# Kernel optimization log

Measured on AMD Instinct MI355X. Metric: run time of the kernel, lower is better.

Reference implementation:

```python
import jax, jax.numpy as jnp
import numpy as np

EPS = 1e-5
NEG_SLOPE = 0.01  # torch F.leaky_relu default


def _batchnorm(h, gamma, beta):
    # BatchNorm1d in training mode: batch stats over node dim, biased variance
    mu = jnp.mean(h, axis=0)
    var = jnp.mean((h - mu) ** 2, axis=0)
    return gamma * (h - mu) * jax.lax.rsqrt(var + EPS) + beta


def setup_inputs() -> dict:
    N, E, H, ED = 16384, 524288, 128, 16
    key = jax.random.key(0)
    ks = jax.random.split(key, 12)
    s = 1.0 / np.sqrt(H)
    return {
        "x": jax.random.normal(ks[0], (N, H), jnp.float32),
        "edge_index": jax.random.randint(ks[1], (2, E), 0, N, jnp.int64),
        "edge_attr": jax.random.normal(ks[2], (E, ED), jnp.float32),
        "Wq": jax.random.normal(ks[3], (H, H), jnp.float32) * s,
        "bq": jnp.zeros((H,), jnp.float32),
        "Wk": jax.random.normal(ks[4], (H, H), jnp.float32) * s,
        "bk": jnp.zeros((H,), jnp.float32),
        "Wv": jax.random.normal(ks[5], (H, H), jnp.float32) * s,
        "bv": jnp.zeros((H,), jnp.float32),
        "We": jax.random.normal(ks[6], (ED, 1), jnp.float32) * (1.0 / np.sqrt(ED)),
        "be": jnp.zeros((1,), jnp.float32),
        "bn1_g": jnp.ones((H,), jnp.float32),
        "bn1_b": jnp.zeros((H,), jnp.float32),
        "W1": jax.random.normal(ks[7], (H, 2 * H), jnp.float32) * s,
        "b1": jnp.zeros((2 * H,), jnp.float32),
        "W2": jax.random.normal(ks[8], (2 * H, H), jnp.float32) * (1.0 / np.sqrt(2 * H)),
        "b2": jnp.zeros((H,), jnp.float32),
        "bn2_g": jnp.ones((H,), jnp.float32),
        "bn2_b": jnp.zeros((H,), jnp.float32),
    }


def reference(x, edge_index, edge_attr, Wq, bq, Wk, bk, Wv, bv, We, be,
              bn1_g, bn1_b, W1, b1, W2, b2, bn2_g, bn2_b):
    N = x.shape[0]
    Q = x @ Wq + bq  # [N, H]
    K = x @ Wk + bk
    V = x @ Wv + bv
    Ebias = (edge_attr @ We + be)[:, 0]  # [E], num_heads == 1
    src, dst = edge_index[0], edge_index[1]
    # per-edge dot product over the FULL hidden dim (as in the source)
    scores = jnp.sum(Q[src] * K[dst], axis=1) + Ebias  # [E]
    scores = jnp.where(scores >= 0, scores, NEG_SLOPE * scores)
    # to_dense_adj scatter-adds edge_attr into a dense [N, N] adjacency
    adj = jnp.zeros((N, N), x.dtype).at[src, dst].add(scores)
    attn = jax.nn.softmax(adj, axis=1)  # dense softmax incl. zero non-edges
    x_new = attn @ V  # [N, H]
    h = _batchnorm(x + x_new, bn1_g, bn1_b)
    ffn = jax.nn.relu(h @ W1 + b1) @ W2 + b2
    return _batchnorm(h + ffn, bn2_g, bn2_b)
```

## Files before the change

kernel.cpp:

```cpp
#include <hip/hip_runtime.h>
#include <hip/hip_bf16.h>
#include <math.h>

#define H 128
#define H2 256
#define SLAB 96
#define LDA 136
#define LDA2 264
#define EPS 1e-5f

typedef __attribute__((ext_vector_type(8))) short s16x8;
typedef __attribute__((ext_vector_type(4))) float f32x4;

__device__ __forceinline__ unsigned short f2bf(float f) {
  unsigned u = __float_as_uint(f);
  unsigned r = (u + 0x7FFFu + ((u >> 16) & 1u)) >> 16;
  return (unsigned short)r;
}
__device__ __forceinline__ float bf2f(unsigned short s) {
  return __uint_as_float(((unsigned)s) << 16);
}
__device__ __forceinline__ unsigned short f2h(float f) {
  union { unsigned short s; _Float16 h; } c; c.h = (_Float16)f; return c.s;
}
__device__ __forceinline__ float h2f(unsigned short u) {
  union { unsigned short s; _Float16 h; } c; c.s = u; return (float)c.h;
}

__global__ void wprep(const float* __restrict__ Wq, const float* __restrict__ Wk,
                      const float* __restrict__ Wv, const float* __restrict__ W1,
                      const float* __restrict__ W2,
                      short* qh, short* kh, short* vh, short* w1h, short* w2h,
                      int* __restrict__ cnt, float* __restrict__ stats, int N)
{
  int job = blockIdx.z;
  if (job == 5) {
    int t = blockIdx.x * 256 + threadIdx.x;
    if (t < N) cnt[t] = 0;
    if (t < 72 * H) stats[t] = 0.f;
    return;
  }
  const float* src; short* dh; int Kd, Nn; bool ashalf;
  if (job == 0)      { src = Wq; dh = qh;  Kd = 128; Nn = 128; ashalf = true; }
  else if (job == 1) { src = Wk; dh = kh;  Kd = 128; Nn = 128; ashalf = true; }
  else if (job == 2) { src = Wv; dh = vh;  Kd = 128; Nn = 128; ashalf = true; }
  else if (job == 3) { src = W1; dh = w1h; Kd = 128; Nn = 256; ashalf = false; }
  else               { src = W2; dh = w2h; Kd = 256; Nn = 128; ashalf = false; }
  int t = blockIdx.x * 256 + threadIdx.x;
  if (t >= Kd * Nn) return;
  int n = t / Kd, k = t - n * Kd;
  float v = src[(size_t)k * Nn + n];
  dh[t] = ashalf ? (short)f2h(v) : (short)f2bf(v);
}

__global__ __launch_bounds__(256) void qkv_mfma(
    const float* __restrict__ x,
    const short* __restrict__ Wqh, const short* __restrict__ Wkh,
    const short* __restrict__ Wvh,
    const float* __restrict__ bq, const float* __restrict__ bk,
    const float* __restrict__ bv,
    unsigned short* __restrict__ Qh, unsigned short* __restrict__ Kh,
    unsigned short* __restrict__ Vh, float* __restrict__ SVp,
    const float* __restrict__ ea, const float* __restrict__ We,
    const float* __restrict__ be, float* __restrict__ Eb,
    int E, int nqkv)
{
  __shared__ __align__(16) short A[64 * LDA];
  int tid = threadIdx.x;

  if (blockIdx.x >= nqkv) {
    int e = (blockIdx.x - nqkv) * 256 + tid;
    if (e < E) {
      float4 w0 = *(const float4*)&We[0], w1 = *(const float4*)&We[4];
      float4 w2 = *(const float4*)&We[8], w3 = *(const float4*)&We[12];
      const float4* p = (const float4*)&ea[(size_t)e * 16];
      float4 a0 = p[0], a1 = p[1], a2 = p[2], a3 = p[3];
      float s = a0.x * w0.x + a0.y * w0.y + a0.z * w0.z + a0.w * w0.w
              + a1.x * w1.x + a1.y * w1.y + a1.z * w1.z + a1.w * w1.w
              + a2.x * w2.x + a2.y * w2.y + a2.z * w2.z + a2.w * w2.w
              + a3.x * w3.x + a3.y * w3.y + a3.z * w3.z + a3.w * w3.w;
      Eb[e] = s + be[0];
    }
    return;
  }

  int bm = blockIdx.x * 64;
  int wave = tid >> 6, lane = tid & 63;
  int quad = lane >> 4, l16 = lane & 15;
  int wn = wave * 32;

#pragma unroll
  for (int i = 0; i < 4; ++i) {
    int g = i * 256 + tid;
    int row = g >> 4, f = g & 15;
    const float4* xp = (const float4*)&x[(size_t)(bm + row) * H + f * 8];
    float4 v0 = xp[0], v1 = xp[1];
    float vv[8] = {v0.x, v0.y, v0.z, v0.w, v1.x, v1.y, v1.z, v1.w};
    s16x8 hv;
#pragma unroll
    for (int j = 0; j < 8; ++j) hv[j] = (short)f2h(vv[j]);
    *(s16x8*)&A[row * LDA + f * 8] = hv;
  }
  __syncthreads();

  for (int ph = 0; ph < 3; ++ph) {
    const short* Bh = (ph == 0) ? Wqh : (ph == 1) ? Wkh : Wvh;

    s16x8 bh[2][4];
#pragma unroll
    for (int nt = 0; nt < 2; ++nt)
#pragma unroll
      for (int ks = 0; ks < 4; ++ks)
        bh[nt][ks] = *(const s16x8*)&Bh[(size_t)(wn + nt * 16 + l16) * H + ks * 32 + quad * 8];

    f32x4 acc[4][2];
#pragma unroll
    for (int mt = 0; mt < 4; ++mt)
#pragma unroll
      for (int nt = 0; nt < 2; ++nt) acc[mt][nt] = (f32x4){0.f, 0.f, 0.f, 0.f};

#pragma unroll
    for (int ks = 0; ks < 4; ++ks) {
      int kof = ks * 32 + quad * 8;
      s16x8 ah[4];
#pragma unroll
      for (int mt = 0; mt < 4; ++mt)
        ah[mt] = *(s16x8*)&A[(mt * 16 + l16) * LDA + kof];
#pragma unroll
      for (int mt = 0; mt < 4; ++mt)
#pragma unroll
        for (int nt = 0; nt < 2; ++nt)
          acc[mt][nt] = __builtin_amdgcn_mfma_f32_16x16x32_f16(ah[mt], bh[nt][ks], acc[mt][nt], 0, 0, 0);
    }

    if (ph == 0) {
#pragma unroll
      for (int nt = 0; nt < 2; ++nt) {
        int col = wn + nt * 16 + l16;
        float bb = bq[col];
#pragma unroll
        for (int mt = 0; mt < 4; ++mt)
#pragma unroll
          for (int r = 0; r < 4; ++r) {
            int row = bm + mt * 16 + quad * 4 + r;
            Qh[(size_t)row * H + col] = f2h(acc[mt][nt][r] + bb);
          }
      }
    } else if (ph == 1) {
#pragma unroll
      for (int nt = 0; nt < 2; ++nt) {
        int col = wn + nt * 16 + l16;
        float bb = bk[col];
#pragma unroll
        for (int mt = 0; mt < 4; ++mt)
#pragma unroll
          for (int r = 0; r < 4; ++r) {
            int row = bm + mt * 16 + quad * 4 + r;
            Kh[(size_t)row * H + col] = f2h(acc[mt][nt][r] + bb);
          }
      }
    } else {
      int bank = blockIdx.x & 7;
#pragma unroll
      for (int nt = 0; nt < 2; ++nt) {
        int col = wn + nt * 16 + l16;
        float bb = bv[col];
        float ps = 0.f;
#pragma unroll
        for (int mt = 0; mt < 4; ++mt)
#pragma unroll
          for (int r = 0; r < 4; ++r) {
            int row = bm + mt * 16 + quad * 4 + r;
            float v = acc[mt][nt][r] + bb;
            Vh[(size_t)row * H + col] = f2h(v);
            ps += v;
          }
        ps += __shfl_xor(ps, 16);
        ps += __shfl_xor(ps, 32);
        if (quad == 0) atomicAdd(&SVp[bank * H + col], ps);
      }
    }
  }
}

__global__ __launch_bounds__(256) void ebfill(
    const int* __restrict__ ei,
    const float* __restrict__ Eb,
    const unsigned short* __restrict__ Qh,
    const unsigned short* __restrict__ Kh,
    int* __restrict__ cnt,
    int2* __restrict__ slabDE, int E, int N)
{
  int tid = threadIdx.x;
  int sub = tid & 7, st = tid >> 3;
  int gsub = blockIdx.x * 32 + st;
  int nsub = gridDim.x * 32;
  const int* eiD = ei + E;

  for (int e = gsub; e < E; e += 2 * nsub) {
    int eA = e, eB = e + nsub;
    bool hasB = (eB < E);
    int sA = ei[eA], dA = eiD[eA];
    float bA = Eb[eA];
    int sB = hasB ? ei[eB] : sA;
    int dB = hasB ? eiD[eB] : dA;
    float bB = hasB ? Eb[eB] : 0.f;

    const s16x8* qpA = (const s16x8*)(Qh + (size_t)sA * H);
    const s16x8* kpA = (const s16x8*)(Kh + (size_t)dA * H);
    const s16x8* qpB = (const s16x8*)(Qh + (size_t)sB * H);
    const s16x8* kpB = (const s16x8*)(Kh + (size_t)dB * H);
    s16x8 qa0 = qpA[sub], qb0 = qpA[8 + sub];
    s16x8 ka0 = kpA[sub], kb0 = kpA[8 + sub];
    s16x8 qa1 = qpB[sub], qb1 = qpB[8 + sub];
    s16x8 ka1 = kpB[sub], kb1 = kpB[8 + sub];
    float s0 = 0.f, s1 = 0.f;
#pragma unroll
    for (int u = 0; u < 8; ++u) {
      s0 += h2f((unsigned short)qa0[u]) * h2f((unsigned short)ka0[u]);
      s0 += h2f((unsigned short)qb0[u]) * h2f((unsigned short)kb0[u]);
      s1 += h2f((unsigned short)qa1[u]) * h2f((unsigned short)ka1[u]);
      s1 += h2f((unsigned short)qb1[u]) * h2f((unsigned short)kb1[u]);
    }
    s0 += __shfl_xor(s0, 1); s1 += __shfl_xor(s1, 1);
    s0 += __shfl_xor(s0, 2); s1 += __shfl_xor(s1, 2);
    s0 += __shfl_xor(s0, 4); s1 += __shfl_xor(s1, 4);
    if (sub == 0) {
      s0 += bA;
      s0 = (s0 >= 0.f) ? s0 : 0.01f * s0;
      int posA = atomicAdd(&cnt[sA], 1);
      if (posA < SLAB) {
        int2 rec; rec.x = dA; rec.y = __float_as_int(s0);
        slabDE[(size_t)sA * SLAB + posA] = rec;
      }
      if (hasB) {
        s1 += bB;
        s1 = (s1 >= 0.f) ? s1 : 0.01f * s1;
        int posB = atomicAdd(&cnt[sB], 1);
        if (posB < SLAB) {
          int2 rec; rec.x = dB; rec.y = __float_as_int(s1);
          slabDE[(size_t)sB * SLAB + posB] = rec;
        }
      }
    }
  }
}

__global__ __launch_bounds__(256) void attn_fused(
    const float* __restrict__ x,
    const unsigned short* __restrict__ Vh,
    const float* __restrict__ SVp, const int* __restrict__ cnt,
    const int2* __restrict__ slabDE,
    float* __restrict__ h1, float* __restrict__ sum1p, float* __restrict__ sq1p,
    int N)
{
  __shared__ float sv[4][SLAB];
  __shared__ int sd[4][SLAB];
  __shared__ short sown[4][SLAB];
  __shared__ int tab[4][128];
  __shared__ float csum[H], csq[H];
  int tid = threadIdx.x;
  int team = tid >> 6, lane = tid & 63;
  int i = blockIdx.x * 4 + team;
  int k = cnt[i]; if (k > SLAB) k = SLAB;
  size_t base = (size_t)i * SLAB;

  if (tid < H) { csum[tid] = 0.f; csq[tid] = 0.f; }
  tab[team][lane] = -1;
  tab[team][lane + 64] = -1;
  __syncthreads();

  for (int p = lane; p < k; p += 64) {
    int2 de = slabDE[base + p];
    sd[team][p] = de.x;
    sv[team][p] = __int_as_float(de.y);
  }

  float2 xx = *(const float2*)&x[(size_t)i * H + lane * 2];
  float sx = 0.f, sy = 0.f;
#pragma unroll
  for (int b = 0; b < 8; ++b) {
    float2 t = *(const float2*)&SVp[b * H + lane * 2];
    sx += t.x; sy += t.y;
  }

  for (int p = lane; p < k; p += 64) {
    int d = sd[team][p];
    unsigned hsh = ((unsigned)d * 2654435761u) >> 25;
    int o;
    while (true) {
      int old = atomicCAS(&tab[team][hsh & 127], -1, p);
      if (old == -1) { o = p; break; }
      if (sd[team][old] == d) { o = old; break; }
      ++hsh;
    }
    sown[team][p] = (short)o;
  }
  for (int p = lane; p < k; p += 64) {
    int o = sown[team][p];
    if (o != p) atomicAdd(&sv[team][o], sv[team][p]);
  }

  float mx = 0.f;
  for (int p = lane; p < k; p += 64)
    if (sown[team][p] == (short)p) mx = fmaxf(mx, sv[team][p]);
#pragma unroll
  for (int msk = 32; msk; msk >>= 1) mx = fmaxf(mx, __shfl_xor(mx, msk));
  float em = __expf(-mx);

  float zl = 0.f;
  for (int p = lane; p < k; p += 64) {
    float cf = 0.f;
    if (sown[team][p] == (short)p) cf = __expf(sv[team][p] - mx) - em;
    sv[team][p] = cf;
    zl += cf;
  }
#pragma unroll
  for (int msk = 32; msk; msk >>= 1) zl += __shfl_xor(zl, msk);
  float Zi = 1.f / ((float)N * em + zl);

  const ushort2* V2 = (const ushort2*)Vh;
  float ax = em * sx, ay = em * sy;
  int c = 0;
  for (; c + 16 <= k; c += 16) {
    float cf[16]; int dd[16]; ushort2 vv[16];
#pragma unroll
    for (int u = 0; u < 16; ++u) { cf[u] = sv[team][c + u]; dd[u] = sd[team][c + u]; }
#pragma unroll
    for (int u = 0; u < 16; ++u) vv[u] = V2[(size_t)dd[u] * 64 + lane];
#pragma unroll
    for (int u = 0; u < 16; ++u) {
      ax += cf[u] * h2f(vv[u].x);
      ay += cf[u] * h2f(vv[u].y);
    }
  }
  for (; c + 8 <= k; c += 8) {
    float cf[8]; int dd[8]; ushort2 vv[8];
#pragma unroll
    for (int u = 0; u < 8; ++u) { cf[u] = sv[team][c + u]; dd[u] = sd[team][c + u]; }
#pragma unroll
    for (int u = 0; u < 8; ++u) vv[u] = V2[(size_t)dd[u] * 64 + lane];
#pragma unroll
    for (int u = 0; u < 8; ++u) {
      ax += cf[u] * h2f(vv[u].x);
      ay += cf[u] * h2f(vv[u].y);
    }
  }
  for (; c < k; ++c) {
    float cf = sv[team][c];
    ushort2 v0 = V2[(size_t)sd[team][c] * 64 + lane];
    ax += cf * h2f(v0.x); ay += cf * h2f(v0.y);
  }
  float ox = xx.x + ax * Zi;
  float oy = xx.y + ay * Zi;
  float2 ov; ov.x = ox; ov.y = oy;
  *(float2*)&h1[(size_t)i * H + lane * 2] = ov;

  int c0 = lane * 2;
  atomicAdd(&csum[c0 + 0], ox); atomicAdd(&csq[c0 + 0], ox * ox);
  atomicAdd(&csum[c0 + 1], oy); atomicAdd(&csq[c0 + 1], oy * oy);
  __syncthreads();
  if (tid < H) {
    int bank = blockIdx.x & 15;
    atomicAdd(&sum1p[bank * H + tid], csum[tid]);
    atomicAdd(&sq1p[bank * H + tid], csq[tid]);
  }
}

__global__ __launch_bounds__(256) void ffn_fused(
    const float* __restrict__ h1, const short* __restrict__ W1h,
    const float* __restrict__ b1, const short* __restrict__ W2h,
    const float* __restrict__ b2,
    const float* __restrict__ sum1p, const float* __restrict__ sq1p,
    const float* __restrict__ g1, const float* __restrict__ bb1,
    float* __restrict__ h2, float* __restrict__ sum2p, float* __restrict__ sq2p,
    float invN)
{
  __shared__ __align__(16) short As[32 * LDA];
  __shared__ __align__(16) short Ts[32 * LDA2];
  __shared__ float aF[H], bF[H];
  int tid = threadIdx.x;
  int bm = blockIdx.x * 32;
  int wave = tid >> 6, lane = tid & 63;
  int quad = lane >> 4, l16 = lane & 15;

  if (tid < H) {
    float s = 0.f, q = 0.f;
#pragma unroll
    for (int b = 0; b < 16; ++b) { s += sum1p[b * H + tid]; q += sq1p[b * H + tid]; }
    float mu = s * invN;
    float var = q * invN - mu * mu;
    float rs = rsqrtf(var + EPS);
    float a = g1[tid] * rs;
    aF[tid] = a;
    bF[tid] = bb1[tid] - a * mu;
  }
  __syncthreads();

  int f = tid & 15;
#pragma unroll
  for (int i = 0; i < 2; ++i) {
    int g = i * 256 + tid;
    int row = g >> 4;
    const float4* xp = (const float4*)&h1[(size_t)(bm + row) * H + f * 8];
    float4 v0 = xp[0], v1 = xp[1];
    float vv[8] = {v0.x, v0.y, v0.z, v0.w, v1.x, v1.y, v1.z, v1.w};
    s16x8 hv;
#pragma unroll
    for (int j = 0; j < 8; ++j) {
      int c = f * 8 + j;
      hv[j] = (short)f2bf(aF[c] * vv[j] + bF[c]);
    }
    *(s16x8*)&As[row * LDA + f * 8] = hv;
  }

  int wn1 = wave * 64;
  s16x8 b1f[4][4];
#pragma unroll
  for (int nt = 0; nt < 4; ++nt)
#pragma unroll
    for (int ks = 0; ks < 4; ++ks)
      b1f[nt][ks] = *(const s16x8*)&W1h[(size_t)(wn1 + nt * 16 + l16) * H + ks * 32 + quad * 8];
  __syncthreads();

  f32x4 acc1[2][4];
#pragma unroll
  for (int mt = 0; mt < 2; ++mt)
#pragma unroll
    for (int nt = 0; nt < 4; ++nt) acc1[mt][nt] = (f32x4){0.f, 0.f, 0.f, 0.f};

#pragma unroll
  for (int ks = 0; ks < 4; ++ks) {
    int kof = ks * 32 + quad * 8;
    s16x8 ah[2];
#pragma unroll
    for (int mt = 0; mt < 2; ++mt) ah[mt] = *(s16x8*)&As[(mt * 16 + l16) * LDA + kof];
#pragma unroll
    for (int mt = 0; mt < 2; ++mt)
#pragma unroll
      for (int nt = 0; nt < 4; ++nt)
        acc1[mt][nt] = __builtin_amdgcn_mfma_f32_16x16x32_bf16(ah[mt], b1f[nt][ks], acc1[mt][nt], 0, 0, 0);
  }

#pragma unroll
  for (int nt = 0; nt < 4; ++nt) {
    int col = wn1 + nt * 16 + l16;
    float bb = b1[col];
#pragma unroll
    for (int mt = 0; mt < 2; ++mt)
#pragma unroll
      for (int r = 0; r < 4; ++r) {
        int row = mt * 16 + quad * 4 + r;
        float v = acc1[mt][nt][r] + bb;
        v = v > 0.f ? v : 0.f;
        Ts[row * LDA2 + col] = (short)f2bf(v);
      }
  }

  int wn2 = wave * 32;
  s16x8 b2f[2][8];
#pragma unroll
  for (int nt = 0; nt < 2; ++nt)
#pragma unroll
    for (int ks = 0; ks < 8; ++ks)
      b2f[nt][ks] = *(const s16x8*)&W2h[(size_t)(wn2 + nt * 16 + l16) * H2 + ks * 32 + quad * 8];
  __syncthreads();

  f32x4 acc2[2][2];
#pragma unroll
  for (int mt = 0; mt < 2; ++mt)
#pragma unroll
    for (int nt = 0; nt < 2; ++nt) acc2[mt][nt] = (f32x4){0.f, 0.f, 0.f, 0.f};

#pragma unroll
  for (int ks = 0; ks < 8; ++ks) {
    int kof = ks * 32 + quad * 8;
    s16x8 ah[2];
#pragma unroll
    for (int mt = 0; mt < 2; ++mt) ah[mt] = *(s16x8*)&Ts[(mt * 16 + l16) * LDA2 + kof];
#pragma unroll
    for (int mt = 0; mt < 2; ++mt)
#pragma unroll
      for (int nt = 0; nt < 2; ++nt)
        acc2[mt][nt] = __builtin_amdgcn_mfma_f32_16x16x32_bf16(ah[mt], b2f[nt][ks], acc2[mt][nt], 0, 0, 0);
  }

  int bank = blockIdx.x & 15;
#pragma unroll
  for (int nt = 0; nt < 2; ++nt) {
    int col = wn2 + nt * 16 + l16;
    float ra = aF[col], rb = bF[col];
    float bb = b2[col];
    float ps = 0.f, pq = 0.f;
#pragma unroll
    for (int mt = 0; mt < 2; ++mt)
#pragma unroll
      for (int r = 0; r < 4; ++r) {
        int row = bm + mt * 16 + quad * 4 + r;
        float rr = ra * h1[(size_t)row * H + col] + rb;
        float v = acc2[mt][nt][r] + bb + rr;
        h2[(size_t)row * H + col] = v;
        ps += v; pq += v * v;
      }
    ps += __shfl_xor(ps, 16); ps += __shfl_xor(ps, 32);
    pq += __shfl_xor(pq, 16); pq += __shfl_xor(pq, 32);
    if (quad == 0) {
      atomicAdd(&sum2p[bank * H + col], ps);
      atomicAdd(&sq2p[bank * H + col], pq);
    }
  }
}

__global__ __launch_bounds__(256) void bn_apply(
    const float* __restrict__ X,
    const float* __restrict__ sum2p, const float* __restrict__ sq2p,
    const float* __restrict__ g2, const float* __restrict__ bb2,
    float* __restrict__ Y, size_t n4, float invN)
{
  __shared__ float A2s[H], B2s[H];
  int tid = threadIdx.x;
  if (tid < H) {
    float s = 0.f, q = 0.f;
#pragma unroll
    for (int b = 0; b < 16; ++b) { s += sum2p[b * H + tid]; q += sq2p[b * H + tid]; }
    float mu = s * invN;
    float var = q * invN - mu * mu;
    float rs = rsqrtf(var + EPS);
    float a = g2[tid] * rs;
    A2s[tid] = a;
    B2s[tid] = bb2[tid] - a * mu;
  }
  __syncthreads();
  size_t i = (size_t)blockIdx.x * blockDim.x + tid;
  if (i >= n4) return;
  float4 v = ((const float4*)X)[i];
  int c = (int)((i * 4) & (H - 1));
  float4 a = *(const float4*)&A2s[c];
  float4 b = *(const float4*)&B2s[c];
  v.x = a.x * v.x + b.x; v.y = a.y * v.y + b.y;
  v.z = a.z * v.z + b.z; v.w = a.w * v.w + b.w;
  ((float4*)Y)[i] = v;
}

extern "C" void kernel_launch(void* const* d_in, const int* in_sizes, int n_in,
                              void* d_out, int out_size, void* d_ws, size_t ws_size,
                              hipStream_t stream)
{
  const float* x  = (const float*)d_in[0];
  const int*   ei = (const int*)d_in[1];
  const float* ea = (const float*)d_in[2];
  const float* Wq = (const float*)d_in[3];
  const float* bq = (const float*)d_in[4];
  const float* Wk = (const float*)d_in[5];
  const float* bk = (const float*)d_in[6];
  const float* Wv = (const float*)d_in[7];
  const float* bv = (const float*)d_in[8];
  const float* We = (const float*)d_in[9];
  const float* be = (const float*)d_in[10];
  const float* g1 = (const float*)d_in[11];
  const float* bb1 = (const float*)d_in[12];
  const float* W1 = (const float*)d_in[13];
  const float* b1 = (const float*)d_in[14];
  const float* W2 = (const float*)d_in[15];
  const float* b2 = (const float*)d_in[16];
  const float* g2 = (const float*)d_in[17];
  const float* bb2 = (const float*)d_in[18];

  int N = in_sizes[0] / H;
  int E = in_sizes[2] / 16;
  size_t NH = (size_t)N * H;
  float invN = 1.0f / (float)N;

  unsigned short* Qh = (unsigned short*)d_ws;
  unsigned short* Kh = Qh + NH;
  unsigned short* Vh = Kh + NH;
  float* h1  = (float*)(Vh + NH);
  int2*  slabDE = (int2*)(h1 + NH);
  int*   cnt    = (int*)(slabDE + (size_t)N * SLAB);
  float* stats  = (float*)(cnt + N);
  float* SVp   = stats;
  float* sum1p = stats + 8 * H;
  float* sq1p  = sum1p + 16 * H;
  float* sum2p = sq1p + 16 * H;
  float* sq2p  = sum2p + 16 * H;
  float* statsEnd = sq2p + 16 * H;
  short* wbuf = (short*)statsEnd;
  short* Wqf = wbuf;
  short* Wkf = Wqf + 16384;
  short* Wvf = Wkf + 16384;
  short* W1h = Wvf + 16384;
  short* W2h = W1h + 32768;
  float* Eb  = (float*)(W2h + 32768);
  float* h2 = (float*)Qh;

  int nqkv = N / 64;
  int nebias = (E + 255) / 256;

  wprep<<<dim3(128, 1, 6), 256, 0, stream>>>(Wq, Wk, Wv, W1, W2,
      Wqf, Wkf, Wvf, W1h, W2h, cnt, stats, N);

  qkv_mfma<<<dim3(nqkv + nebias), 256, 0, stream>>>(
      x, Wqf, Wkf, Wvf, bq, bk, bv, Qh, Kh, Vh, SVp,
      ea, We, be, Eb, E, nqkv);

  ebfill<<<dim3(2048), 256, 0, stream>>>(ei, Eb, Qh, Kh, cnt, slabDE, E, N);

  attn_fused<<<dim3(N / 4), 256, 0, stream>>>(x, Vh, SVp, cnt, slabDE,
                                              h1, sum1p, sq1p, N);

  ffn_fused<<<dim3(N / 32), 256, 0, stream>>>(h1, W1h, b1, W2h, b2,
      sum1p, sq1p, g1, bb1, h2, sum2p, sq2p, invN);

  bn_apply<<<dim3((int)((NH / 4 + 255) / 256)), 256, 0, stream>>>(
      h2, sum2p, sq2p, g2, bb2, (float*)d_out, NH / 4, invN);
}
```

Baseline: 222.0 us.

## Fold edge bucketing into QKV kernel and compute QK scores inside attention

The separate ebfill kernel is removed. The edge-bias blocks of the QKV kernel now bucket each edge by source into the per-row slab with the raw bias. The attention kernel then computes the Q·K dot product and leaky-ReLU for each slab entry, loading the row's Q vector once and reusing it across all its edges. This removes a kernel launch, the Eb intermediate buffer and repeated per-edge Q gathers. In exchange, the attention kernel does more work per row and has to wait on the K-row gathers itself.

```diff
diff --git a/kernel.cpp b/kernel.cpp
--- a/kernel.cpp
+++ b/kernel.cpp
@@ -62,7 +62,8 @@
     unsigned short* __restrict__ Qh, unsigned short* __restrict__ Kh,
     unsigned short* __restrict__ Vh, float* __restrict__ SVp,
     const float* __restrict__ ea, const float* __restrict__ We,
-    const float* __restrict__ be, float* __restrict__ Eb,
+    const float* __restrict__ be, const int* __restrict__ ei,
+    int* __restrict__ cnt, int2* __restrict__ slabDE,
     int E, int nqkv)
 {
   __shared__ __align__(16) short A[64 * LDA];
@@ -79,7 +80,14 @@
               + a1.x * w1.x + a1.y * w1.y + a1.z * w1.z + a1.w * w1.w
               + a2.x * w2.x + a2.y * w2.y + a2.z * w2.z + a2.w * w2.w
               + a3.x * w3.x + a3.y * w3.y + a3.z * w3.z + a3.w * w3.w;
-      Eb[e] = s + be[0];
+      s += be[0];
+      int src = ei[e];
+      int dst = ei[E + e];
+      int pos = atomicAdd(&cnt[src], 1);
+      if (pos < SLAB) {
+        int2 rec; rec.x = dst; rec.y = __float_as_int(s);
+        slabDE[(size_t)src * SLAB + pos] = rec;
+      }
     }
     return;
   }
@@ -183,71 +191,10 @@
   }
 }
 
-__global__ __launch_bounds__(256) void ebfill(
-    const int* __restrict__ ei,
-    const float* __restrict__ Eb,
+__global__ __launch_bounds__(256) void attn_fused(
+    const float* __restrict__ x,
     const unsigned short* __restrict__ Qh,
     const unsigned short* __restrict__ Kh,
-    int* __restrict__ cnt,
-    int2* __restrict__ slabDE, int E, int N)
-{
-  int tid = threadIdx.x;
-  int sub = tid & 7, st = tid >> 3;
-  int gsub = blockIdx.x * 32 + st;
-  int nsub = gridDim.x * 32;
-  const int* eiD = ei + E;
-
-  for (int e = gsub; e < E; e += 2 * nsub) {
-    int eA = e, eB = e + nsub;
-    bool hasB = (eB < E);
-    int sA = ei[eA], dA = eiD[eA];
-    float bA = Eb[eA];
-    int sB = hasB ? ei[eB] : sA;
-    int dB = hasB ? eiD[eB] : dA;
-    float bB = hasB ? Eb[eB] : 0.f;
-
-    const s16x8* qpA = (const s16x8*)(Qh + (size_t)sA * H);
-    const s16x8* kpA = (const s16x8*)(Kh + (size_t)dA * H);
-    const s16x8* qpB = (const s16x8*)(Qh + (size_t)sB * H);
-    const s16x8* kpB = (const s16x8*)(Kh + (size_t)dB * H);
-    s16x8 qa0 = qpA[sub], qb0 = qpA[8 + sub];
-    s16x8 ka0 = kpA[sub], kb0 = kpA[8 + sub];
-    s16x8 qa1 = qpB[sub], qb1 = qpB[8 + sub];
-    s16x8 ka1 = kpB[sub], kb1 = kpB[8 + sub];
-    float s0 = 0.f, s1 = 0.f;
-#pragma unroll
-    for (int u = 0; u < 8; ++u) {
-      s0 += h2f((unsigned short)qa0[u]) * h2f((unsigned short)ka0[u]);
-      s0 += h2f((unsigned short)qb0[u]) * h2f((unsigned short)kb0[u]);
-      s1 += h2f((unsigned short)qa1[u]) * h2f((unsigned short)ka1[u]);
-      s1 += h2f((unsigned short)qb1[u]) * h2f((unsigned short)kb1[u]);
-    }
-    s0 += __shfl_xor(s0, 1); s1 += __shfl_xor(s1, 1);
-    s0 += __shfl_xor(s0, 2); s1 += __shfl_xor(s1, 2);
-    s0 += __shfl_xor(s0, 4); s1 += __shfl_xor(s1, 4);
-    if (sub == 0) {
-      s0 += bA;
-      s0 = (s0 >= 0.f) ? s0 : 0.01f * s0;
-      int posA = atomicAdd(&cnt[sA], 1);
-      if (posA < SLAB) {
-        int2 rec; rec.x = dA; rec.y = __float_as_int(s0);
-        slabDE[(size_t)sA * SLAB + posA] = rec;
-      }
-      if (hasB) {
-        s1 += bB;
-        s1 = (s1 >= 0.f) ? s1 : 0.01f * s1;
-        int posB = atomicAdd(&cnt[sB], 1);
-        if (posB < SLAB) {
-          int2 rec; rec.x = dB; rec.y = __float_as_int(s1);
-          slabDE[(size_t)sB * SLAB + posB] = rec;
-        }
-      }
-    }
-  }
-}
-
-__global__ __launch_bounds__(256) void attn_fused(
-    const float* __restrict__ x,
     const unsigned short* __restrict__ Vh,
     const float* __restrict__ SVp, const int* __restrict__ cnt,
     const int2* __restrict__ slabDE,
@@ -282,6 +229,58 @@
   for (int b = 0; b < 8; ++b) {
     float2 t = *(const float2*)&SVp[b * H + lane * 2];
     sx += t.x; sy += t.y;
+  }
+
+  int sub = lane & 7, slot = lane >> 3;
+  const s16x8* qp = (const s16x8*)(Qh + (size_t)i * H);
+  s16x8 qa = qp[sub], qb = qp[8 + sub];
+  if (k > 0) {
+    int c = 0;
+    for (; c + 16 <= k; c += 16) {
+      int p0 = c + slot, p1 = c + 8 + slot;
+      int d0 = sd[team][p0], d1 = sd[team][p1];
+      const s16x8* k0 = (const s16x8*)(Kh + (size_t)d0 * H);
+      const s16x8* k1 = (const s16x8*)(Kh + (size_t)d1 * H);
+      s16x8 ka0 = k0[sub], kb0 = k0[8 + sub];
+      s16x8 ka1 = k1[sub], kb1 = k1[8 + sub];
+      float s0 = 0.f, s1 = 0.f;
+#pragma unroll
+      for (int u = 0; u < 8; ++u) {
+        s0 += h2f((unsigned short)qa[u]) * h2f((unsigned short)ka0[u]);
+        s0 += h2f((unsigned short)qb[u]) * h2f((unsigned short)kb0[u]);
+        s1 += h2f((unsigned short)qa[u]) * h2f((unsigned short)ka1[u]);
+        s1 += h2f((unsigned short)qb[u]) * h2f((unsigned short)kb1[u]);
+      }
+      s0 += __shfl_xor(s0, 1); s1 += __shfl_xor(s1, 1);
+      s0 += __shfl_xor(s0, 2); s1 += __shfl_xor(s1, 2);
+      s0 += __shfl_xor(s0, 4); s1 += __shfl_xor(s1, 4);
+      if (sub == 0) {
+        float ss0 = s0 + sv[team][p0];
+        sv[team][p0] = (ss0 >= 0.f) ? ss0 : 0.01f * ss0;
+        float ss1 = s1 + sv[team][p1];
+        sv[team][p1] = (ss1 >= 0.f) ? ss1 : 0.01f * ss1;
+      }
+    }
+    for (; c < k; c += 8) {
+      int p = c + slot;
+      int pc = (p < k) ? p : 0;
+      int d = sd[team][pc];
+      const s16x8* kp = (const s16x8*)(Kh + (size_t)d * H);
+      s16x8 ka = kp[sub], kb = kp[8 + sub];
+      float s = 0.f;
+#pragma unroll
+      for (int u = 0; u < 8; ++u) {
+        s += h2f((unsigned short)qa[u]) * h2f((unsigned short)ka[u]);
+        s += h2f((unsigned short)qb[u]) * h2f((unsigned short)kb[u]);
+      }
+      s += __shfl_xor(s, 1);
+      s += __shfl_xor(s, 2);
+      s += __shfl_xor(s, 4);
+      if (sub == 0 && p < k) {
+        float ss = s + sv[team][p];
+        sv[team][p] = (ss >= 0.f) ? ss : 0.01f * ss;
+      }
+    }
   }
 
   for (int p = lane; p < k; p += 64) {
@@ -590,22 +589,19 @@
   short* Wvf = Wkf + 16384;
   short* W1h = Wvf + 16384;
   short* W2h = W1h + 32768;
-  float* Eb  = (float*)(W2h + 32768);
   float* h2 = (float*)Qh;
 
   int nqkv = N / 64;
-  int nebias = (E + 255) / 256;
+  int nscat = (E + 255) / 256;
 
   wprep<<<dim3(128, 1, 6), 256, 0, stream>>>(Wq, Wk, Wv, W1, W2,
       Wqf, Wkf, Wvf, W1h, W2h, cnt, stats, N);
 
-  qkv_mfma<<<dim3(nqkv + nebias), 256, 0, stream>>>(
+  qkv_mfma<<<dim3(nqkv + nscat), 256, 0, stream>>>(
       x, Wqf, Wkf, Wvf, bq, bk, bv, Qh, Kh, Vh, SVp,
-      ea, We, be, Eb, E, nqkv);
-
-  ebfill<<<dim3(2048), 256, 0, stream>>>(ei, Eb, Qh, Kh, cnt, slabDE, E, N);
-
-  attn_fused<<<dim3(N / 4), 256, 0, stream>>>(x, Vh, SVp, cnt, slabDE,
+      ea, We, be, ei, cnt, slabDE, E, nqkv);
+
+  attn_fused<<<dim3(N / 4), 256, 0, stream>>>(x, Qh, Kh, Vh, SVp, cnt, slabDE,
                                               h1, sum1p, sq1p, N);
 
   ffn_fused<<<dim3(N / 32), 256, 0, stream>>>(h1, W1h, b1, W2h, b2,
```

New measurement: 220.8 us. About the same (-0.5%).
